# Performance work log

Hardware: AMD Instinct MI355X
Metric: run time of the kernel (lower is better)

Reference implementation:

```python
import jax, jax.numpy as jnp
import numpy as np

DIM = 256
FFN = 1024
T = 32768
EPS = 1e-6  # flax LayerNorm default


def layernorm(x, g, b):
    mu = jnp.mean(x, axis=-1, keepdims=True)
    var = jnp.mean(jnp.square(x - mu), axis=-1, keepdims=True)
    return (x - mu) * jax.lax.rsqrt(var + EPS) * g + b


def setup_inputs() -> dict:
    key = jax.random.key(0)
    ks = jax.random.split(key, 16)
    s = lambda k, shape, fan: jax.random.normal(k, shape, jnp.float32) * (1.0 / np.sqrt(fan))
    return {
        "xs": jax.random.normal(ks[0], (T, DIM), jnp.float32),
        "h0": jax.random.normal(ks[1], (DIM,), jnp.float32) * 0.01,  # normal() init
        "Wi": s(ks[2], (DIM, 3 * DIM), DIM),   # input kernels [ir|iz|in], no bias (flax GRUCell)
        "Wh": s(ks[3], (DIM, 3 * DIM), DIM),   # recurrent kernels [hr|hz|hn]
        "bh": jnp.zeros((3 * DIM,), jnp.float32),
        "Wg": s(ks[4], (DIM, DIM), DIM),       # GRU block output Dense
        "bg": jnp.zeros((DIM,), jnp.float32),
        "g1": jnp.ones((DIM,), jnp.float32),
        "be1": jnp.zeros((DIM,), jnp.float32),
        "W1": s(ks[5], (DIM, FFN), DIM),       # FFN l1
        "b1": jnp.zeros((FFN,), jnp.float32),
        "W2": s(ks[6], (FFN, DIM), FFN),       # FFN l2
        "b2": jnp.zeros((DIM,), jnp.float32),
        "g2": jnp.ones((DIM,), jnp.float32),
        "be2": jnp.zeros((DIM,), jnp.float32),
    }


def reference(xs, h0, Wi, Wh, bh, Wg, bg, g1, be1, W1, b1, W2, b2, g2, be2):
    # --- GRU block (flax GRUCell: r,z,n gates; input dense has no bias) ---
    xg = xs @ Wi  # [T, 3*DIM], precompute input projections for all steps

    def step(h, xg_t):
        hg = h @ Wh + bh
        xr, xz, xn = jnp.split(xg_t, 3)
        hr, hz, hn = jnp.split(hg, 3)
        r = jax.nn.sigmoid(xr + hr)
        z = jax.nn.sigmoid(xz + hz)
        n = jnp.tanh(xn + r * hn)
        h_new = (1.0 - z) * n + z * h
        return h_new, h_new

    _, ys = jax.lax.scan(step, h0, xg)  # ys: [T, DIM]
    y = layernorm(xs + jax.nn.relu(ys) @ Wg + bg, g1, be1)
    # --- FeedForward block (dropout_rate=0 -> identity) ---
    out = layernorm(y + jax.nn.relu(y @ W1 + b1) @ W2 + b2, g2, be2)
    return out
```

## Files before the change

### kernel.cpp

```cpp
#include <hip/hip_runtime.h>
#include <hip/hip_bf16.h>
#include <hip/hip_fp16.h>

#define T_LEN 32768
#define NDIM 256
#define NFFN 1024

typedef __attribute__((ext_vector_type(8))) short bf8v;
typedef __attribute__((ext_vector_type(4))) float f4v;
typedef __attribute__((ext_vector_type(4))) int   i4v;
typedef _Float16 fp16_t;

__device__ __forceinline__ unsigned short f2bf(float f) {
  union { float f; unsigned int i; } v; v.f = f;
  unsigned int u = v.i;
  u += 0x7FFFu + ((u >> 16) & 1u);
  return (unsigned short)(u >> 16);
}

__device__ __forceinline__ bf8v load_frag(const unsigned short* base, int ld, int r0, int k0) {
  int lane = threadIdx.x & 63;
  const unsigned short* p = base + (size_t)(r0 + (lane & 15)) * ld + (k0 + ((lane >> 4) << 3));
  return *(const bf8v*)p;
}
__device__ __forceinline__ bf8v load_frag_f32(const float* base, int ld, int r0, int k0) {
  int lane = threadIdx.x & 63;
  const float* p = base + (size_t)(r0 + (lane & 15)) * ld + (k0 + ((lane >> 4) << 3));
  float4 u = *(const float4*)p;
  float4 v = *(const float4*)(p + 4);
  bf8v r;
  r[0] = (short)f2bf(u.x); r[1] = (short)f2bf(u.y); r[2] = (short)f2bf(u.z); r[3] = (short)f2bf(u.w);
  r[4] = (short)f2bf(v.x); r[5] = (short)f2bf(v.y); r[6] = (short)f2bf(v.z); r[7] = (short)f2bf(v.w);
  return r;
}

__global__ __launch_bounds__(256) void k_tr_bf(const float* __restrict__ src,
                                               unsigned short* __restrict__ dst, int K, int N) {
  int idx = blockIdx.x * 256 + threadIdx.x;
  if (idx >= K * N) return;
  int k = idx / N, n = idx - k * N;
  dst[n * K + k] = f2bf(src[idx]);
}

__global__ __launch_bounds__(64) void k_prep(const float* __restrict__ Wh,
                                             char* __restrict__ WhQ,
                                             float* __restrict__ F) {
  int j = blockIdx.x, t = threadIdx.x;
  float w[4]; float m = 0.f;
#pragma unroll
  for (int i = 0; i < 4; ++i) {
    w[i] = Wh[(size_t)(t + 64 * i) * 768 + j];
    m = fmaxf(m, fabsf(w[i]));
  }
#pragma unroll
  for (int off = 32; off >= 1; off >>= 1) m = fmaxf(m, __shfl_xor(m, off));
  float mm = fmaxf(m, 1e-20f);
  float inv = 127.f / mm;
#pragma unroll
  for (int i = 0; i < 4; ++i) {
    int qv = (int)rintf(w[i] * inv);
    WhQ[(size_t)j * 256 + t + 64 * i] = (char)qv;
  }
  if (t == 0) F[j] = mm * (1.f / (127.f * 127.f));
}

__global__ __launch_bounds__(256) void k_xg(const float* __restrict__ xs,
                                            const unsigned short* __restrict__ WiT,
                                            __half* __restrict__ xg) {
  int mt = blockIdx.x, ns = blockIdx.y;
  int wave = threadIdx.x >> 6, lane = threadIdx.x & 63;
  int r0 = mt * 16;
  f4v acc[4];
#pragma unroll
  for (int i = 0; i < 4; ++i) acc[i] = (f4v){0.f, 0.f, 0.f, 0.f};
#pragma unroll
  for (int kc = 0; kc < 256; kc += 32) {
    bf8v a = load_frag_f32(xs, NDIM, r0, kc);
#pragma unroll
    for (int nt = 0; nt < 4; ++nt) {
      int c0 = ns * 256 + wave * 64 + nt * 16;
      bf8v b = load_frag(WiT, NDIM, c0, kc);
      acc[nt] = __builtin_amdgcn_mfma_f32_16x16x32_bf16(a, b, acc[nt], 0, 0, 0);
    }
  }
#pragma unroll
  for (int nt = 0; nt < 4; ++nt) {
    int col = ns * 256 + wave * 64 + nt * 16 + (lane & 15);
    int rb = r0 + ((lane >> 4) << 2);
#pragma unroll
    for (int r = 0; r < 4; ++r)
      xg[(size_t)(rb + r) * 768 + col] = (__half)acc[nt][r];
  }
}

__global__ __launch_bounds__(512, 2) void k_gru(const char* __restrict__ WhQ,
                                                const float* __restrict__ F,
                                                const float* __restrict__ bh,
                                                const float* __restrict__ h0,
                                                const __half* __restrict__ xg,
                                                unsigned short* __restrict__ relu_ys) {
  __shared__ __align__(16) char hbuf[2][256];
  const int tid = threadIdx.x;
  const int w = tid >> 6, lane = tid & 63;
  const int c = lane & 15, copy = lane >> 4;
  const int jA = 32 * w + c, jB = jA + 16;
  const int sel = copy & 1;
  const int jX = sel ? jB : jA;
  const bool writer = (copy < 2);

  int cbs[6] = { 32 * w, 32 * w + 16, 256 + 32 * w, 256 + 32 * w + 16,
                 512 + 32 * w, 512 + 32 * w + 16 };
  i4v BQ[6][4];
#pragma unroll
  for (int ti = 0; ti < 6; ++ti) {
    const i4v* p = (const i4v*)(WhQ + (size_t)(cbs[ti] + c) * 256 + copy * 16);
#pragma unroll
    for (int kt = 0; kt < 4; ++kt)
      BQ[ti][kt] = p[kt * 4];
  }

  float Fr = F[jX], Fz = F[256 + jX], Fn = F[512 + jX];
  float bhr = bh[jX], bhz = bh[256 + jX], bhn = bh[512 + jX];
  float h = h0[jX];
  if (writer) {
    int q = max(-127, min(127, (int)rintf(h * 127.f)));
    hbuf[0][jX] = (char)q;
  }
  float xr = (float)xg[jX], xz = (float)xg[256 + jX], xn = (float)xg[512 + jX];
  float prev_relu = 0.f;
  __syncthreads();

  for (int t = 0; t < T_LEN; ++t) {
    const int p = t & 1;
    i4v acc[6];
#pragma unroll
    for (int i = 0; i < 6; ++i) acc[i] = (i4v){0, 0, 0, 0};
#pragma unroll
    for (int kt = 0; kt < 4; ++kt) {
      i4v a = *(const i4v*)(&hbuf[p][kt * 64 + copy * 16]);
#pragma unroll
      for (int ti = 0; ti < 6; ++ti)
        acc[ti] = __builtin_amdgcn_mfma_i32_16x16x64_i8(a, BQ[ti][kt], acc[ti], 0, 0, 0);
    }

    if (t > 0 && writer)
      relu_ys[(size_t)(t - 1) * NDIM + jX] = f2bf(prev_relu);
    const __half* row = xg + (size_t)((t + 1) & (T_LEN - 1)) * 768;
    float nxr = (float)row[jX];
    float nxz = (float)row[256 + jX];
    float nxn = (float)row[512 + jX];

    int ai_r = sel ? acc[1][0] : acc[0][0];
    int ai_z = sel ? acc[3][0] : acc[2][0];
    int ai_n = sel ? acc[5][0] : acc[4][0];
    float hr = (float)ai_r * Fr + bhr;
    float hz = (float)ai_z * Fz + bhz;
    float hn = (float)ai_n * Fn + bhn;
    float r = 1.f / (1.f + __expf(-(xr + hr)));
    float z = 1.f / (1.f + __expf(-(xz + hz)));
    float ar = xn + r * hn;
    float e = __expf(-2.f * fabsf(ar));
    float th = copysignf((1.f - e) / (1.f + e), ar);
    h = (1.f - z) * th + z * h;

    if (writer) {
      int q = max(-127, min(127, (int)rintf(h * 127.f)));
      hbuf[p ^ 1][jX] = (char)q;
    }
    prev_relu = fmaxf(h, 0.f);
    xr = nxr; xz = nxz; xn = nxn;
    __syncthreads();
  }
  if (writer)
    relu_ys[(size_t)(T_LEN - 1) * NDIM + jX] = f2bf(prev_relu);
}

__global__ __launch_bounds__(256) void k_res_ln1(const unsigned short* __restrict__ rys,
                                                 const unsigned short* __restrict__ WgT,
                                                 const float* __restrict__ xs,
                                                 const float* __restrict__ bg,
                                                 const float* __restrict__ g1,
                                                 const float* __restrict__ be1,
                                                 float* __restrict__ y) {
  __shared__ float sbuf[16][264];
  int mt = blockIdx.x, tid = threadIdx.x;
  int wave = tid >> 6, lane = tid & 63;
  int r0 = mt * 16;
  f4v acc[4];
#pragma unroll
  for (int i = 0; i < 4; ++i) acc[i] = (f4v){0.f, 0.f, 0.f, 0.f};
#pragma unroll
  for (int kc = 0; kc < 256; kc += 32) {
    bf8v a = load_frag(rys, NDIM, r0, kc);
#pragma unroll
    for (int nt = 0; nt < 4; ++nt) {
      bf8v b = load_frag(WgT, NDIM, wave * 64 + nt * 16, kc);
      acc[nt] = __builtin_amdgcn_mfma_f32_16x16x32_bf16(a, b, acc[nt], 0, 0, 0);
    }
  }
#pragma unroll
  for (int nt = 0; nt < 4; ++nt) {
    int col = wave * 64 + nt * 16 + (lane & 15);
    int rl = ((lane >> 4) << 2);
#pragma unroll
    for (int r = 0; r < 4; ++r)
      sbuf[rl + r][col] = acc[nt][r] + xs[(size_t)(r0 + rl + r) * NDIM + col] + bg[col];
  }
  __syncthreads();
  int rr = tid >> 4, c0 = tid & 15;
  float sum = 0.f, sq = 0.f;
#pragma unroll
  for (int m = 0; m < 16; ++m) {
    float v = sbuf[rr][c0 + 16 * m];
    sum += v; sq += v * v;
  }
#pragma unroll
  for (int o = 1; o < 16; o <<= 1) {
    sum += __shfl_xor(sum, o, 16);
    sq  += __shfl_xor(sq, o, 16);
  }
  float mu = sum * (1.f / 256.f);
  float var = sq * (1.f / 256.f) - mu * mu;
  float rs = rsqrtf(var + 1e-6f);
#pragma unroll
  for (int m = 0; m < 16; ++m) {
    int col = c0 + 16 * m;
    float v = (sbuf[rr][col] - mu) * rs * g1[col] + be1[col];
    y[(size_t)(r0 + rr) * NDIM + col] = v;
  }
}

__global__ __launch_bounds__(256) void k_ffn(const float* __restrict__ y,
                                             const unsigned short* __restrict__ W1T,
                                             const float* __restrict__ b1,
                                             const unsigned short* __restrict__ W2T,
                                             const float* __restrict__ b2,
                                             const float* __restrict__ g2,
                                             const float* __restrict__ be2,
                                             float* __restrict__ out) {
  __shared__ unsigned short hidb[16][1032];
  __shared__ float sbuf[16][264];
  int mt = blockIdx.x, tid = threadIdx.x;
  int wave = tid >> 6, lane = tid & 63;
  int r0 = mt * 16;

  f4v acc1[16];
#pragma unroll
  for (int i = 0; i < 16; ++i) acc1[i] = (f4v){0.f, 0.f, 0.f, 0.f};
#pragma unroll
  for (int kc = 0; kc < 256; kc += 32) {
    bf8v a = load_frag_f32(y, NDIM, r0, kc);
#pragma unroll
    for (int nt = 0; nt < 16; ++nt) {
      bf8v b = load_frag(W1T, NDIM, wave * 256 + nt * 16, kc);
      acc1[nt] = __builtin_amdgcn_mfma_f32_16x16x32_bf16(a, b, acc1[nt], 0, 0, 0);
    }
  }
#pragma unroll
  for (int nt = 0; nt < 16; ++nt) {
    int col = wave * 256 + nt * 16 + (lane & 15);
    int rl = ((lane >> 4) << 2);
#pragma unroll
    for (int r = 0; r < 4; ++r)
      hidb[rl + r][col] = f2bf(fmaxf(acc1[nt][r] + b1[col], 0.f));
  }
  __syncthreads();

  f4v acc2[4];
#pragma unroll
  for (int i = 0; i < 4; ++i) acc2[i] = (f4v){0.f, 0.f, 0.f, 0.f};
  for (int kc = 0; kc < 1024; kc += 32) {
    bf8v a = *(const bf8v*)(&hidb[lane & 15][kc + ((lane >> 4) << 3)]);
#pragma unroll
    for (int nt = 0; nt < 4; ++nt) {
      bf8v b = load_frag(W2T, NFFN, wave * 64 + nt * 16, kc);
      acc2[nt] = __builtin_amdgcn_mfma_f32_16x16x32_bf16(a, b, acc2[nt], 0, 0, 0);
    }
  }
#pragma unroll
  for (int nt = 0; nt < 4; ++nt) {
    int col = wave * 64 + nt * 16 + (lane & 15);
    int rl = ((lane >> 4) << 2);
#pragma unroll
    for (int r = 0; r < 4; ++r)
      sbuf[rl + r][col] = acc2[nt][r] + y[(size_t)(r0 + rl + r) * NDIM + col] + b2[col];
  }
  __syncthreads();
  int rr = tid >> 4, c0 = tid & 15;
  float sum = 0.f, sq = 0.f;
#pragma unroll
  for (int m = 0; m < 16; ++m) {
    float v = sbuf[rr][c0 + 16 * m];
    sum += v; sq += v * v;
  }
#pragma unroll
  for (int o = 1; o < 16; o <<= 1) {
    sum += __shfl_xor(sum, o, 16);
    sq  += __shfl_xor(sq, o, 16);
  }
  float mu = sum * (1.f / 256.f);
  float var = sq * (1.f / 256.f) - mu * mu;
  float rs = rsqrtf(var + 1e-6f);
#pragma unroll
  for (int m = 0; m < 16; ++m) {
    int col = c0 + 16 * m;
    float v = (sbuf[rr][col] - mu) * rs * g2[col] + be2[col];
    out[(size_t)(r0 + rr) * NDIM + col] = v;
  }
}

extern "C" void kernel_launch(void* const* d_in, const int* in_sizes, int n_in,
                              void* d_out, int out_size, void* d_ws, size_t ws_size,
                              hipStream_t stream) {
  const float* xs  = (const float*)d_in[0];
  const float* h0  = (const float*)d_in[1];
  const float* Wi  = (const float*)d_in[2];
  const float* Wh  = (const float*)d_in[3];
  const float* bh  = (const float*)d_in[4];
  const float* Wg  = (const float*)d_in[5];
  const float* bg  = (const float*)d_in[6];
  const float* g1  = (const float*)d_in[7];
  const float* be1 = (const float*)d_in[8];
  const float* W1  = (const float*)d_in[9];
  const float* b1  = (const float*)d_in[10];
  const float* W2  = (const float*)d_in[11];
  const float* b2  = (const float*)d_in[12];
  const float* g2  = (const float*)d_in[13];
  const float* be2 = (const float*)d_in[14];

  char* ws = (char*)d_ws;
  __half* xg = (__half*)(ws + 0);
  float*  yb = (float*)(ws + 0);
  unsigned short* rys = (unsigned short*)(ws + 50331648);
  unsigned short* WiT = (unsigned short*)(ws + 67108864);
  char*           WhQ = (char*)          (ws + 67502080);
  float*          Fsc = (float*)         (ws + 67698688);
  unsigned short* WgT = (unsigned short*)(ws + 67895296);
  unsigned short* W1T = (unsigned short*)(ws + 68026368);
  unsigned short* W2T = (unsigned short*)(ws + 68550656);

  k_tr_bf<<<(256 * 768 + 255) / 256, 256, 0, stream>>>(Wi, WiT, 256, 768);
  k_tr_bf<<<(256 * 256 + 255) / 256, 256, 0, stream>>>(Wg, WgT, 256, 256);
  k_tr_bf<<<(256 * 1024 + 255) / 256, 256, 0, stream>>>(W1, W1T, 256, 1024);
  k_tr_bf<<<(1024 * 256 + 255) / 256, 256, 0, stream>>>(W2, W2T, 1024, 256);
  k_prep<<<768, 64, 0, stream>>>(Wh, WhQ, Fsc);

  k_xg<<<dim3(T_LEN / 16, 3), 256, 0, stream>>>(xs, WiT, xg);
  k_gru<<<1, 512, 0, stream>>>(WhQ, Fsc, bh, h0, xg, rys);
  k_res_ln1<<<T_LEN / 16, 256, 0, stream>>>(rys, WgT, xs, bg, g1, be1, yb);
  k_ffn<<<T_LEN / 16, 256, 0, stream>>>(yb, W1T, b1, W2T, b2, g2, be2, (float*)d_out);
}
```

Before: 22.90 ms.

## Transpose GRU input gates to time-major columns and batch-prefetch eight steps

The input-projection output is now stored transposed (gate column by time), so each GRU thread loads eight timesteps of its gate inputs with one 16-byte load per gate, prefetched one block ahead. This replaces three scattered scalar loads on every serial step. The inner step loop is unrolled by eight, and the first MFMA of each step takes a zero accumulator instead of a separately zeroed one. relu(ys) and Wg are switched from bf16 to fp16, so the residual GEMM uses the f16 MFMA.

```diff
diff --git a/kernel.cpp b/kernel.cpp
--- a/kernel.cpp
+++ b/kernel.cpp
@@ -7,6 +7,7 @@
 #define NFFN 1024
 
 typedef __attribute__((ext_vector_type(8))) short bf8v;
+typedef __attribute__((ext_vector_type(8))) _Float16 h8v;
 typedef __attribute__((ext_vector_type(4))) float f4v;
 typedef __attribute__((ext_vector_type(4))) int   i4v;
 typedef _Float16 fp16_t;
@@ -16,6 +17,9 @@
   unsigned int u = v.i;
   u += 0x7FFFu + ((u >> 16) & 1u);
   return (unsigned short)(u >> 16);
+}
+__device__ __forceinline__ h8v as_h8(bf8v x) {
+  union { bf8v b; h8v h; } u; u.b = x; return u.h;
 }
 
 __device__ __forceinline__ bf8v load_frag(const unsigned short* base, int ld, int r0, int k0) {
@@ -41,6 +45,13 @@
   int k = idx / N, n = idx - k * N;
   dst[n * K + k] = f2bf(src[idx]);
 }
+__global__ __launch_bounds__(256) void k_tr_h(const float* __restrict__ src,
+                                              fp16_t* __restrict__ dst, int K, int N) {
+  int idx = blockIdx.x * 256 + threadIdx.x;
+  if (idx >= K * N) return;
+  int k = idx / N, n = idx - k * N;
+  dst[n * K + k] = (fp16_t)src[idx];
+}
 
 __global__ __launch_bounds__(64) void k_prep(const float* __restrict__ Wh,
                                              char* __restrict__ WhQ,
@@ -66,7 +77,7 @@
 
 __global__ __launch_bounds__(256) void k_xg(const float* __restrict__ xs,
                                             const unsigned short* __restrict__ WiT,
-                                            __half* __restrict__ xg) {
+                                            fp16_t* __restrict__ xgT) {
   int mt = blockIdx.x, ns = blockIdx.y;
   int wave = threadIdx.x >> 6, lane = threadIdx.x & 63;
   int r0 = mt * 16;
@@ -87,9 +98,10 @@
   for (int nt = 0; nt < 4; ++nt) {
     int col = ns * 256 + wave * 64 + nt * 16 + (lane & 15);
     int rb = r0 + ((lane >> 4) << 2);
-#pragma unroll
-    for (int r = 0; r < 4; ++r)
-      xg[(size_t)(rb + r) * 768 + col] = (__half)acc[nt][r];
+    union { int2 v; fp16_t h[4]; } pk;
+    pk.h[0] = (fp16_t)acc[nt][0]; pk.h[1] = (fp16_t)acc[nt][1];
+    pk.h[2] = (fp16_t)acc[nt][2]; pk.h[3] = (fp16_t)acc[nt][3];
+    *(int2*)(xgT + (size_t)col * T_LEN + rb) = pk.v;
   }
 }
 
@@ -97,8 +109,8 @@
                                                 const float* __restrict__ F,
                                                 const float* __restrict__ bh,
                                                 const float* __restrict__ h0,
-                                                const __half* __restrict__ xg,
-                                                unsigned short* __restrict__ relu_ys) {
+                                                const fp16_t* __restrict__ xgT,
+                                                fp16_t* __restrict__ relu_ys) {
   __shared__ __align__(16) char hbuf[2][256];
   const int tid = threadIdx.x;
   const int w = tid >> 6, lane = tid & 63;
@@ -118,6 +130,7 @@
     for (int kt = 0; kt < 4; ++kt)
       BQ[ti][kt] = p[kt * 4];
   }
+  const i4v IZERO = (i4v){0, 0, 0, 0};
 
   float Fr = F[jX], Fz = F[256 + jX], Fn = F[512 + jX];
   float bhr = bh[jX], bhz = bh[256 + jX], bhn = bh[512 + jX];
@@ -126,53 +139,72 @@
     int q = max(-127, min(127, (int)rintf(h * 127.f)));
     hbuf[0][jX] = (char)q;
   }
-  float xr = (float)xg[jX], xz = (float)xg[256 + jX], xn = (float)xg[512 + jX];
+  const fp16_t* xrp = xgT + (size_t)jX * T_LEN;
+  const fp16_t* xzp = xgT + (size_t)(256 + jX) * T_LEN;
+  const fp16_t* xnp = xgT + (size_t)(512 + jX) * T_LEN;
+  union U8h { int4 v; fp16_t e[8]; };
+  U8h cr, cz, cn;
+  cr.v = *(const int4*)(xrp);
+  cz.v = *(const int4*)(xzp);
+  cn.v = *(const int4*)(xnp);
   float prev_relu = 0.f;
   __syncthreads();
 
-  for (int t = 0; t < T_LEN; ++t) {
-    const int p = t & 1;
-    i4v acc[6];
-#pragma unroll
-    for (int i = 0; i < 6; ++i) acc[i] = (i4v){0, 0, 0, 0};
-#pragma unroll
-    for (int kt = 0; kt < 4; ++kt) {
-      i4v a = *(const i4v*)(&hbuf[p][kt * 64 + copy * 16]);
-#pragma unroll
-      for (int ti = 0; ti < 6; ++ti)
-        acc[ti] = __builtin_amdgcn_mfma_i32_16x16x64_i8(a, BQ[ti][kt], acc[ti], 0, 0, 0);
-    }
-
-    if (t > 0 && writer)
-      relu_ys[(size_t)(t - 1) * NDIM + jX] = f2bf(prev_relu);
-    const __half* row = xg + (size_t)((t + 1) & (T_LEN - 1)) * 768;
-    float nxr = (float)row[jX];
-    float nxz = (float)row[256 + jX];
-    float nxn = (float)row[512 + jX];
-
-    int ai_r = sel ? acc[1][0] : acc[0][0];
-    int ai_z = sel ? acc[3][0] : acc[2][0];
-    int ai_n = sel ? acc[5][0] : acc[4][0];
-    float hr = (float)ai_r * Fr + bhr;
-    float hz = (float)ai_z * Fz + bhz;
-    float hn = (float)ai_n * Fn + bhn;
-    float r = 1.f / (1.f + __expf(-(xr + hr)));
-    float z = 1.f / (1.f + __expf(-(xz + hz)));
-    float ar = xn + r * hn;
-    float e = __expf(-2.f * fabsf(ar));
-    float th = copysignf((1.f - e) / (1.f + e), ar);
-    h = (1.f - z) * th + z * h;
-
-    if (writer) {
-      int q = max(-127, min(127, (int)rintf(h * 127.f)));
-      hbuf[p ^ 1][jX] = (char)q;
-    }
-    prev_relu = fmaxf(h, 0.f);
-    xr = nxr; xz = nxz; xn = nxn;
-    __syncthreads();
+  for (int tb = 0; tb < T_LEN; tb += 8) {
+    const int tn = (tb + 8) & (T_LEN - 1);
+    U8h nr, nz, nn2;
+    nr.v  = *(const int4*)(xrp + tn);
+    nz.v  = *(const int4*)(xzp + tn);
+    nn2.v = *(const int4*)(xnp + tn);
+#pragma unroll
+    for (int tt = 0; tt < 8; ++tt) {
+      const int t = tb + tt;
+      const int p = tt & 1;
+      i4v acc[6];
+      {
+        i4v a0 = *(const i4v*)(&hbuf[p][copy * 16]);
+#pragma unroll
+        for (int ti = 0; ti < 6; ++ti)
+          acc[ti] = __builtin_amdgcn_mfma_i32_16x16x64_i8(a0, BQ[ti][0], IZERO, 0, 0, 0);
+      }
+#pragma unroll
+      for (int kt = 1; kt < 4; ++kt) {
+        i4v a = *(const i4v*)(&hbuf[p][kt * 64 + copy * 16]);
+#pragma unroll
+        for (int ti = 0; ti < 6; ++ti)
+          acc[ti] = __builtin_amdgcn_mfma_i32_16x16x64_i8(a, BQ[ti][kt], acc[ti], 0, 0, 0);
+      }
+
+      if ((tt > 0 || tb > 0) && writer)
+        relu_ys[(size_t)(t - 1) * NDIM + jX] = (fp16_t)prev_relu;
+      float xr = (float)cr.e[tt];
+      float xz = (float)cz.e[tt];
+      float xn = (float)cn.e[tt];
+
+      int ai_r = sel ? acc[1][0] : acc[0][0];
+      int ai_z = sel ? acc[3][0] : acc[2][0];
+      int ai_n = sel ? acc[5][0] : acc[4][0];
+      float hr = (float)ai_r * Fr + bhr;
+      float hz = (float)ai_z * Fz + bhz;
+      float hn = (float)ai_n * Fn + bhn;
+      float r = 1.f / (1.f + __expf(-(xr + hr)));
+      float z = 1.f / (1.f + __expf(-(xz + hz)));
+      float ar = xn + r * hn;
+      float e = __expf(-2.f * fabsf(ar));
+      float th = copysignf((1.f - e) / (1.f + e), ar);
+      h = (1.f - z) * th + z * h;
+
+      if (writer) {
+        int q = max(-127, min(127, (int)rintf(h * 127.f)));
+        hbuf[p ^ 1][jX] = (char)q;
+      }
+      prev_relu = fmaxf(h, 0.f);
+      __syncthreads();
+    }
+    cr = nr; cz = nz; cn = nn2;
   }
   if (writer)
-    relu_ys[(size_t)(T_LEN - 1) * NDIM + jX] = f2bf(prev_relu);
+    relu_ys[(size_t)(T_LEN - 1) * NDIM + jX] = (fp16_t)prev_relu;
 }
 
 __global__ __launch_bounds__(256) void k_res_ln1(const unsigned short* __restrict__ rys,
@@ -191,11 +223,11 @@
   for (int i = 0; i < 4; ++i) acc[i] = (f4v){0.f, 0.f, 0.f, 0.f};
 #pragma unroll
   for (int kc = 0; kc < 256; kc += 32) {
-    bf8v a = load_frag(rys, NDIM, r0, kc);
+    h8v a = as_h8(load_frag(rys, NDIM, r0, kc));
 #pragma unroll
     for (int nt = 0; nt < 4; ++nt) {
-      bf8v b = load_frag(WgT, NDIM, wave * 64 + nt * 16, kc);
-      acc[nt] = __builtin_amdgcn_mfma_f32_16x16x32_bf16(a, b, acc[nt], 0, 0, 0);
+      h8v b = as_h8(load_frag(WgT, NDIM, wave * 64 + nt * 16, kc));
+      acc[nt] = __builtin_amdgcn_mfma_f32_16x16x32_f16(a, b, acc[nt], 0, 0, 0);
     }
   }
 #pragma unroll
@@ -329,24 +361,25 @@
   const float* be2 = (const float*)d_in[14];
 
   char* ws = (char*)d_ws;
-  __half* xg = (__half*)(ws + 0);
-  float*  yb = (float*)(ws + 0);
-  unsigned short* rys = (unsigned short*)(ws + 50331648);
+  fp16_t* xgT = (fp16_t*)(ws + 0);
+  float*  yb  = (float*)(ws + 0);
+  fp16_t* rys = (fp16_t*)(ws + 50331648);
   unsigned short* WiT = (unsigned short*)(ws + 67108864);
   char*           WhQ = (char*)          (ws + 67502080);
   float*          Fsc = (float*)         (ws + 67698688);
-  unsigned short* WgT = (unsigned short*)(ws + 67895296);
+  fp16_t*         WgT = (fp16_t*)        (ws + 67895296);
   unsigned short* W1T = (unsigned short*)(ws + 68026368);
   unsigned short* W2T = (unsigned short*)(ws + 68550656);
 
   k_tr_bf<<<(256 * 768 + 255) / 256, 256, 0, stream>>>(Wi, WiT, 256, 768);
-  k_tr_bf<<<(256 * 256 + 255) / 256, 256, 0, stream>>>(Wg, WgT, 256, 256);
+  k_tr_h <<<(256 * 256 + 255) / 256, 256, 0, stream>>>(Wg, WgT, 256, 256);
   k_tr_bf<<<(256 * 1024 + 255) / 256, 256, 0, stream>>>(W1, W1T, 256, 1024);
   k_tr_bf<<<(1024 * 256 + 255) / 256, 256, 0, stream>>>(W2, W2T, 1024, 256);
   k_prep<<<768, 64, 0, stream>>>(Wh, WhQ, Fsc);
 
-  k_xg<<<dim3(T_LEN / 16, 3), 256, 0, stream>>>(xs, WiT, xg);
-  k_gru<<<1, 512, 0, stream>>>(WhQ, Fsc, bh, h0, xg, rys);
-  k_res_ln1<<<T_LEN / 16, 256, 0, stream>>>(rys, WgT, xs, bg, g1, be1, yb);
+  k_xg<<<dim3(T_LEN / 16, 3), 256, 0, stream>>>(xs, WiT, xgT);
+  k_gru<<<1, 512, 0, stream>>>(WhQ, Fsc, bh, h0, xgT, rys);
+  k_res_ln1<<<T_LEN / 16, 256, 0, stream>>>((const unsigned short*)rys, (const unsigned short*)WgT,
+                                            xs, bg, g1, be1, yb);
   k_ffn<<<T_LEN / 16, 256, 0, stream>>>(yb, W1T, b1, W2T, b2, g2, be2, (float*)d_out);
 }
```

After: 20.92 ms. 8.6% less time.
